# Kernel optimization log

Measured on AMD Instinct MI355X. Metric: run time of the kernel, lower is better.

## Reference

```python
import jax, jax.numpy as jnp
import numpy as np

N = 20000      # nodes
E = 160000     # edges (before self loops)
F = 256        # num_features
HID = 64       # hidden_channels
H = 4          # num_heads
HC = HID // H  # head channels = 16
C = 10         # num_classes
K = 3          # hops
ALPHA = 0.1
CST = 1e-5


def setup_inputs() -> dict:
    key = jax.random.key(0)
    ks = jax.random.split(key, 12)
    node_feat = jax.random.normal(ks[0], (N, F), dtype=jnp.float32)
    edge_index = jax.random.randint(ks[1], (2, E), 0, N, dtype=jnp.int32)

    def lin(k, fan_in, fan_out):
        b = 1.0 / np.sqrt(fan_in)
        kw, kb = jax.random.split(k)
        W = jax.random.uniform(kw, (fan_in, fan_out), jnp.float32, -b, b)
        bias = jax.random.uniform(kb, (fan_out,), jnp.float32, -b, b)
        return W, bias

    W_in, b_in = lin(ks[2], F, HID)
    Wq, bq = lin(ks[3], HID, H * HC)
    Wk, bk = lin(ks[4], HID, H * HC)
    Wv, bv = lin(ks[5], HID, H * C)
    W_out, b_out = lin(ks[6], H * C, C)

    # hopwise: alpha*(1-alpha)^k, last entry (1-alpha)^K
    hw = ALPHA * (1 - ALPHA) ** np.arange(K + 1, dtype=np.float32)
    hw[-1] = (1 - ALPHA) ** K
    hopwise = jnp.asarray(hw, dtype=jnp.float32)
    # temp: uniform one-head vector normalized by L1, tiled per head
    bound = np.sqrt(3.0 / (K + 1))
    onehead = jax.random.uniform(ks[7], (K + 1,), jnp.float32, -bound, bound)
    onehead = onehead / jnp.sum(jnp.abs(onehead))
    temp = jnp.tile(onehead[None, :], (H, 1))  # [H, K+1]

    return dict(node_feat=node_feat, edge_index=edge_index, W_in=W_in, b_in=b_in,
                Wq=Wq, bq=bq, Wk=Wk, bk=bk, Wv=Wv, bv=bv,
                W_out=W_out, b_out=b_out, hopwise=hopwise, temp=temp)


def reference(node_feat, edge_index, W_in, b_in, Wq, bq, Wk, bk, Wv, bv,
              W_out, b_out, hopwise, temp):
    # add self loops
    loops = jnp.arange(N, dtype=edge_index.dtype)
    ei = jnp.concatenate([edge_index, jnp.stack([loops, loops])], axis=1)
    row, col = ei[0], ei[1]
    # symmetric-normalized laplacian weights
    deg = jnp.zeros((N,), node_feat.dtype).at[col].add(1.0)
    dis = jnp.where(deg > 0, 1.0 / jnp.sqrt(jnp.maximum(deg, 1.0)), 0.0)
    norm = dis[row] * dis[col]  # [E+N]

    x = jax.nn.relu(node_feat @ W_in + b_in)                      # [N, HID]
    Q = (1.0 + jax.nn.elu(x @ Wq + bq)).reshape(N, H, HC)
    Kt = (1.0 + jax.nn.elu(x @ Wk + bk)).reshape(N, H, HC)
    V = (x @ Wv + bv).reshape(N, H, C)

    M = jnp.einsum('nhi,nhj->nhij', Kt, V)                        # [N, H, HC, C]
    hidden = V * hopwise[0]
    # NOTE: faithful to torch: softmax over dim=-2 of temp [H, K+1] == head axis
    layerwise = jax.nn.softmax(temp, axis=0)                      # [H, K+1]

    for hop in range(K):
        M = jax.ops.segment_sum(norm[:, None, None, None] * M[row], col, num_segments=N)
        Kt = jax.ops.segment_sum(norm[:, None, None] * Kt[row], col, num_segments=N)
        Hh = jnp.einsum('nhi,nhij->nhj', Q, M)                    # [N, H, C]
        Cd = jnp.einsum('nhi,nhi->nh', Q, Kt)[..., None] + CST    # [N, H, 1]
        gamma = hopwise[hop + 1] * layerwise[:, hop + 1][:, None]  # [H, 1]
        hidden = hidden + gamma * (Hh / Cd)

    out = hidden.reshape(N, H * C) @ W_out + b_out                # [N, C]
    return out
```

## Files before the change

### kernel.cpp

```cpp
#include <hip/hip_runtime.h>
#include <stdint.h>

#define kN   20000
#define kE   160000
#define kET  (kN + kE)
#define kF   256
#define kHID 64
#define kH   4
#define kHC  16
#define kC   10
#define kK   3
#define kCST 1e-5f
#define kBN  32
#define kNB  ((kN + 255) / 256)

__device__ __forceinline__ uint16_t f2bf(float x) {
    uint32_t u = __float_as_uint(x);
    u += 0x7fffu + ((u >> 16) & 1u);
    return (uint16_t)(u >> 16);
}
__device__ __forceinline__ float lo16(uint32_t p) { return __uint_as_float(p << 16); }
__device__ __forceinline__ float hi16(uint32_t p) { return __uint_as_float(p & 0xffff0000u); }
__device__ __forceinline__ uint32_t pack2(float a, float b) {
    return ((uint32_t)f2bf(b) << 16) | (uint32_t)f2bf(a);
}

__global__ void deg_kernel(const int* __restrict__ ei, int* __restrict__ deg) {
    int e = blockIdx.x * blockDim.x + threadIdx.x;
    if (e >= kET) return;
    int c = (e < kE) ? ei[kE + e] : (e - kE);
    atomicAdd(&deg[c], 1);
}

__global__ __launch_bounds__(256) void degsum_kernel(const int* __restrict__ deg,
                                                     int* __restrict__ partial) {
    __shared__ int sw[4];
    int t = threadIdx.x;
    int idx = blockIdx.x * 256 + t;
    int v = (idx < kN) ? deg[idx] : 0;
#pragma unroll
    for (int off = 32; off >= 1; off >>= 1) v += __shfl_xor(v, off, 64);
    if ((t & 63) == 0) sw[t >> 6] = v;
    __syncthreads();
    if (t == 0) partial[blockIdx.x] = sw[0] + sw[1] + sw[2] + sw[3];
}

__global__ __launch_bounds__(128) void midscan_kernel(
    const int* __restrict__ partial, int* __restrict__ offsets,
    const float* __restrict__ hopwise, const float* __restrict__ temp,
    float* __restrict__ gammas) {
    __shared__ int ws0;
    int t = threadIdx.x;
    int v = (t < kNB) ? partial[t] : 0;
    int incl = v;
#pragma unroll
    for (int off = 1; off < 64; off <<= 1) {
        int u = __shfl_up(incl, off, 64);
        if ((t & 63) >= off) incl += u;
    }
    if (t == 63) ws0 = incl;
    __syncthreads();
    int add = (t >= 64) ? ws0 : 0;
    if (t < kNB) offsets[t] = add + incl - v;
    if (t == 0) {
        for (int k = 1; k <= kK; ++k) {
            float mx = -1e30f;
            for (int h = 0; h < kH; ++h) mx = fmaxf(mx, temp[h * (kK + 1) + k]);
            float ex[kH]; float sum = 0.f;
            for (int h = 0; h < kH; ++h) { ex[h] = __expf(temp[h * (kK + 1) + k] - mx); sum += ex[h]; }
            for (int h = 0; h < kH; ++h) gammas[(k - 1) * kH + h] = hopwise[k] * ex[h] / sum;
        }
    }
}

__global__ __launch_bounds__(256) void ptrw_kernel(const int* __restrict__ deg,
                                                   const int* __restrict__ offsets,
                                                   int* __restrict__ ptr) {
    __shared__ int sw[4];
    int t = threadIdx.x;
    int idx = blockIdx.x * 256 + t;
    int v = (idx < kN) ? deg[idx] : 0;
    int incl = v;
#pragma unroll
    for (int off = 1; off < 64; off <<= 1) {
        int u = __shfl_up(incl, off, 64);
        if ((t & 63) >= off) incl += u;
    }
    int wid = t >> 6;
    if ((t & 63) == 63) sw[wid] = incl;
    __syncthreads();
    int wadd = 0;
    for (int j = 0; j < 4; ++j) wadd += (j < wid) ? sw[j] : 0;
    int excl = offsets[blockIdx.x] + wadd + incl - v;
    if (idx < kN) ptr[idx] = excl;
    if (idx == kN - 1) ptr[kN] = excl + v;
}

__global__ void scatter_kernel(const int* __restrict__ ei, const int* __restrict__ deg,
                               const int* __restrict__ ptr, int* __restrict__ cursor,
                               int* __restrict__ src, float* __restrict__ wgt) {
    int e = blockIdx.x * blockDim.x + threadIdx.x;
    if (e >= kET) return;
    int r, c;
    if (e < kE) { r = ei[e]; c = ei[kE + e]; } else { r = c = e - kE; }
    float wv = rsqrtf((float)deg[r]) * rsqrtf((float)deg[c]);
    int pos = ptr[c] + atomicAdd(&cursor[c], 1);
    src[pos] = r;
    wgt[pos] = wv;
}

__global__ __launch_bounds__(256) void proj_kernel(
    const float* __restrict__ feat, const float* __restrict__ W_in, const float* __restrict__ b_in,
    const float* __restrict__ Wq, const float* __restrict__ bq,
    const float* __restrict__ Wk, const float* __restrict__ bk,
    const float* __restrict__ Wv, const float* __restrict__ bv,
    const float* __restrict__ hopwise,
    float* __restrict__ Qg, float* __restrict__ Ktg, float* __restrict__ hidden,
    float* __restrict__ Vg) {
    __shared__ float sF[kBN * 68];
    __shared__ float sW[64 * 68];
    __shared__ float sX[kBN * 68];

    int t = threadIdx.x;
    int tx = t & 15, ty = t >> 4;
    int n0 = blockIdx.x * kBN;
    int r0 = ty * 2, r1 = ty * 2 + 1;

    float acc[2][4];
#pragma unroll
    for (int i = 0; i < 2; ++i)
#pragma unroll
        for (int j = 0; j < 4; ++j) acc[i][j] = 0.f;

    for (int ks = 0; ks < 4; ++ks) {
        int k0 = ks * 64;
#pragma unroll
        for (int i = 0; i < 2; ++i) {
            int slot = t + 256 * i;
            int row = slot >> 4, cg = slot & 15;
            *(float4*)&sF[row * 68 + cg * 4] =
                *(const float4*)&feat[(size_t)(n0 + row) * kF + k0 + cg * 4];
        }
#pragma unroll
        for (int i = 0; i < 4; ++i) {
            int slot = t + 256 * i;
            int row = slot >> 4, cg = slot & 15;
            *(float4*)&sW[row * 68 + cg * 4] =
                *(const float4*)&W_in[(size_t)(k0 + row) * kHID + cg * 4];
        }
        __syncthreads();
#pragma unroll 8
        for (int kk = 0; kk < 64; ++kk) {
            float4 b = *(float4*)&sW[kk * 68 + tx * 4];
            float a0 = sF[r0 * 68 + kk], a1 = sF[r1 * 68 + kk];
            acc[0][0] += a0 * b.x; acc[0][1] += a0 * b.y;
            acc[0][2] += a0 * b.z; acc[0][3] += a0 * b.w;
            acc[1][0] += a1 * b.x; acc[1][1] += a1 * b.y;
            acc[1][2] += a1 * b.z; acc[1][3] += a1 * b.w;
        }
        __syncthreads();
    }
    {
        float bb[4];
#pragma unroll
        for (int j = 0; j < 4; ++j) bb[j] = b_in[tx * 4 + j];
#pragma unroll
        for (int i = 0; i < 2; ++i) {
            float4 xr;
            xr.x = fmaxf(acc[i][0] + bb[0], 0.f);
            xr.y = fmaxf(acc[i][1] + bb[1], 0.f);
            xr.z = fmaxf(acc[i][2] + bb[2], 0.f);
            xr.w = fmaxf(acc[i][3] + bb[3], 0.f);
            *(float4*)&sX[(r0 + i) * 68 + tx * 4] = xr;
        }
    }
#pragma unroll
    for (int i = 0; i < 4; ++i) {
        int slot = t + 256 * i;
        int row = slot >> 4, cg = slot & 15;
        *(float4*)&sW[row * 68 + cg * 4] = *(const float4*)&Wq[(size_t)row * kHID + cg * 4];
    }
    __syncthreads();

    float qa[2][4];
#pragma unroll
    for (int i = 0; i < 2; ++i)
#pragma unroll
        for (int j = 0; j < 4; ++j) qa[i][j] = 0.f;
#pragma unroll 8
    for (int kk = 0; kk < 64; ++kk) {
        float4 b = *(float4*)&sW[kk * 68 + tx * 4];
        float a0 = sX[r0 * 68 + kk], a1 = sX[r1 * 68 + kk];
        qa[0][0] += a0 * b.x; qa[0][1] += a0 * b.y;
        qa[0][2] += a0 * b.z; qa[0][3] += a0 * b.w;
        qa[1][0] += a1 * b.x; qa[1][1] += a1 * b.y;
        qa[1][2] += a1 * b.z; qa[1][3] += a1 * b.w;
    }
    {
        float bqv[4];
#pragma unroll
        for (int j = 0; j < 4; ++j) bqv[j] = bq[tx * 4 + j];
#pragma unroll
        for (int i = 0; i < 2; ++i) {
            float4 qv;
            float q0 = qa[i][0] + bqv[0], q1 = qa[i][1] + bqv[1];
            float q2 = qa[i][2] + bqv[2], q3 = qa[i][3] + bqv[3];
            qv.x = (q0 > 0.f) ? 1.f + q0 : __expf(q0);
            qv.y = (q1 > 0.f) ? 1.f + q1 : __expf(q1);
            qv.z = (q2 > 0.f) ? 1.f + q2 : __expf(q2);
            qv.w = (q3 > 0.f) ? 1.f + q3 : __expf(q3);
            *(float4*)&Qg[(size_t)(n0 + r0 + i) * kHID + tx * 4] = qv;
        }
    }
    __syncthreads();
#pragma unroll
    for (int i = 0; i < 4; ++i) {
        int slot = t + 256 * i;
        int row = slot >> 4, cg = slot & 15;
        *(float4*)&sW[row * 68 + cg * 4] = *(const float4*)&Wk[(size_t)row * kHID + cg * 4];
    }
    __syncthreads();

    float ka[2][4];
#pragma unroll
    for (int i = 0; i < 2; ++i)
#pragma unroll
        for (int j = 0; j < 4; ++j) ka[i][j] = 0.f;
#pragma unroll 8
    for (int kk = 0; kk < 64; ++kk) {
        float4 b = *(float4*)&sW[kk * 68 + tx * 4];
        float a0 = sX[r0 * 68 + kk], a1 = sX[r1 * 68 + kk];
        ka[0][0] += a0 * b.x; ka[0][1] += a0 * b.y;
        ka[0][2] += a0 * b.z; ka[0][3] += a0 * b.w;
        ka[1][0] += a1 * b.x; ka[1][1] += a1 * b.y;
        ka[1][2] += a1 * b.z; ka[1][3] += a1 * b.w;
    }
    {
        float bkv[4];
#pragma unroll
        for (int j = 0; j < 4; ++j) bkv[j] = bk[tx * 4 + j];
#pragma unroll
        for (int i = 0; i < 2; ++i) {
            float4 kv;
            float k0v = ka[i][0] + bkv[0], k1v = ka[i][1] + bkv[1];
            float k2v = ka[i][2] + bkv[2], k3v = ka[i][3] + bkv[3];
            kv.x = (k0v > 0.f) ? 1.f + k0v : __expf(k0v);
            kv.y = (k1v > 0.f) ? 1.f + k1v : __expf(k1v);
            kv.z = (k2v > 0.f) ? 1.f + k2v : __expf(k2v);
            kv.w = (k3v > 0.f) ? 1.f + k3v : __expf(k3v);
            *(float4*)&Ktg[(size_t)(n0 + r0 + i) * kHID + tx * 4] = kv;
        }
    }
    __syncthreads();
#pragma unroll
    for (int i = 0; i < 3; ++i) {
        int slot = t + 256 * i;
        if (slot < 640) {
            int row = slot / 10, cg = slot % 10;
            *(float4*)&sW[row * 44 + cg * 4] = *(const float4*)&Wv[(size_t)row * 40 + cg * 4];
        }
    }
    __syncthreads();

    if (t < 160) {
        int txv = t % 10, tyv = t / 10;
        int vr0 = tyv * 2;
        float va[2][4];
#pragma unroll
        for (int i = 0; i < 2; ++i)
#pragma unroll
            for (int j = 0; j < 4; ++j) va[i][j] = 0.f;
#pragma unroll 8
        for (int kk = 0; kk < 64; ++kk) {
            float4 b = *(float4*)&sW[kk * 44 + txv * 4];
            float a0 = sX[vr0 * 68 + kk], a1 = sX[(vr0 + 1) * 68 + kk];
            va[0][0] += a0 * b.x; va[0][1] += a0 * b.y;
            va[0][2] += a0 * b.z; va[0][3] += a0 * b.w;
            va[1][0] += a1 * b.x; va[1][1] += a1 * b.y;
            va[1][2] += a1 * b.z; va[1][3] += a1 * b.w;
        }
        float bvv[4];
#pragma unroll
        for (int j = 0; j < 4; ++j) bvv[j] = bv[txv * 4 + j];
        float hw0 = hopwise[0];
#pragma unroll
        for (int i = 0; i < 2; ++i) {
            int row = vr0 + i;
            float4 vr;
            vr.x = va[i][0] + bvv[0]; vr.y = va[i][1] + bvv[1];
            vr.z = va[i][2] + bvv[2]; vr.w = va[i][3] + bvv[3];
            *(float4*)&Vg[(size_t)(n0 + row) * 40 + txv * 4] = vr;
            float4 hr;
            hr.x = vr.x * hw0; hr.y = vr.y * hw0; hr.z = vr.z * hw0; hr.w = vr.w * hw0;
            *(float4*)&hidden[(size_t)(n0 + row) * 40 + txv * 4] = hr;
        }
    }
}

__global__ __launch_bounds__(256) void hop0_kernel(
    const int* __restrict__ ptr, const int* __restrict__ src, const float* __restrict__ wgt,
    const float* __restrict__ Ktin, const float* __restrict__ Vin,
    const float* __restrict__ Q,
    uint16_t* __restrict__ Mout, float* __restrict__ Ktout,
    float* __restrict__ hidden, const float* __restrict__ gammas) {
    __shared__ float Ml[4][640];
    __shared__ float Ktl[4][64];
    __shared__ float Ql[4][64];
    int w = threadIdx.x >> 6;
    int l = threadIdx.x & 63;
    int n = blockIdx.x * 4 + w;
    int beg = ptr[n], end = ptr[n + 1];

    Ql[w][l] = Q[(size_t)n * 64 + l];

    int base_v = 10 * (l >> 4);
    int vidx = (l < 40) ? l : l - 40;

    float m[10];
#pragma unroll
    for (int i = 0; i < 10; ++i) m[i] = 0.f;
    float kacc = 0.f;

    auto edge = [&](float kl, float vv, float wv) {
        float kw = wv * kl;
        kacc += wv * kl;
#pragma unroll
        for (int c = 0; c < 10; ++c) {
            float vc = __shfl(vv, base_v + c, 64);
            m[c] += kw * vc;
        }
    };

    int e = beg;
    for (; e + 4 <= end; e += 4) {
        int s0 = src[e], s1 = src[e + 1], s2 = src[e + 2], s3 = src[e + 3];
        float w0 = wgt[e], w1 = wgt[e + 1], w2 = wgt[e + 2], w3 = wgt[e + 3];
        float ka = Ktin[(size_t)s0 * 64 + l], va = Vin[(size_t)s0 * 40 + vidx];
        float kb = Ktin[(size_t)s1 * 64 + l], vb = Vin[(size_t)s1 * 40 + vidx];
        float kc = Ktin[(size_t)s2 * 64 + l], vc = Vin[(size_t)s2 * 40 + vidx];
        float kd = Ktin[(size_t)s3 * 64 + l], vd = Vin[(size_t)s3 * 40 + vidx];
        edge(ka, va, w0); edge(kb, vb, w1); edge(kc, vc, w2); edge(kd, vd, w3);
    }
    for (; e < end; ++e) {
        int s0 = src[e];
        edge(Ktin[(size_t)s0 * 64 + l], Vin[(size_t)s0 * 40 + vidx], wgt[e]);
    }

    {
        uint32_t* orow = (uint32_t*)Mout + (size_t)n * 320 + 5 * l;
        orow[0] = pack2(m[0], m[1]);
        orow[1] = pack2(m[2], m[3]);
        orow[2] = pack2(m[4], m[5]);
        orow[3] = pack2(m[6], m[7]);
        orow[4] = pack2(m[8], m[9]);
        Ktout[(size_t)n * 64 + l] = kacc;
    }
#pragma unroll
    for (int c = 0; c < 10; c += 2)
        *(float2*)&Ml[w][10 * l + c] = make_float2(m[c], m[c + 1]);
    Ktl[w][l] = kacc;
    __syncthreads();

    int tt = threadIdx.x;
    if (tt < 160) {
        int ww = tt / 40, o = tt % 40;
        int h = o / 10, j = o % 10;
        const float* q  = &Ql[ww][h * 16];
        const float* kk = &Ktl[ww][h * 16];
        const float* mm = &Ml[ww][h * 160 + j];
        float cd = kCST, hh = 0.f;
#pragma unroll
        for (int i = 0; i < 16; ++i) { cd += q[i] * kk[i]; hh += q[i] * mm[i * 10]; }
        int nn = blockIdx.x * 4 + ww;
        hidden[(size_t)nn * 40 + o] += gammas[h] * hh / cd;
    }
}

template<bool LAST>
__global__ __launch_bounds__(256) void hop2_kernel(
    const int* __restrict__ ptr, const int* __restrict__ src, const float* __restrict__ wgt,
    const uint16_t* __restrict__ Min, uint16_t* __restrict__ Mout,
    const float* __restrict__ Ktin, float* __restrict__ Ktout,
    const float* __restrict__ Q, float* __restrict__ hidden,
    const float* __restrict__ gammas,
    const float* __restrict__ W_out, const float* __restrict__ b_out,
    float* __restrict__ out) {
    __shared__ float Ml[4][640];
    __shared__ float Ktl[4][64];
    __shared__ float Ql[4][64];
    __shared__ float Hl[4][40];
    int w = threadIdx.x >> 6;
    int l = threadIdx.x & 63;
    int n = blockIdx.x * 4 + w;
    int beg = ptr[n], end = ptr[n + 1];
    const uint32_t* Mw = (const uint32_t*)Min;

    Ql[w][l] = Q[(size_t)n * 64 + l];

    float m0=0,m1=0,m2=0,m3=0,m4=0,m5=0,m6=0,m7=0,m8=0,m9=0;
    float kacc = 0.f;
    int e = beg;
    for (; e + 4 <= end; e += 4) {
        int s0 = src[e], s1 = src[e + 1], s2 = src[e + 2], s3 = src[e + 3];
        float w0 = wgt[e], w1 = wgt[e + 1], w2 = wgt[e + 2], w3 = wgt[e + 3];
        const uint32_t* p0 = Mw + (size_t)s0 * 320 + l;
        const uint32_t* p1 = Mw + (size_t)s1 * 320 + l;
        const uint32_t* p2 = Mw + (size_t)s2 * 320 + l;
        const uint32_t* p3 = Mw + (size_t)s3 * 320 + l;
        uint32_t a0 = p0[0], a1 = p0[64], a2 = p0[128], a3 = p0[192], a4 = p0[256];
        uint32_t b0 = p1[0], b1 = p1[64], b2 = p1[128], b3 = p1[192], b4 = p1[256];
        uint32_t c0 = p2[0], c1 = p2[64], c2 = p2[128], c3 = p2[192], c4 = p2[256];
        uint32_t d0 = p3[0], d1 = p3[64], d2 = p3[128], d3 = p3[192], d4 = p3[256];
        float ka = Ktin[(size_t)s0 * 64 + l], kb = Ktin[(size_t)s1 * 64 + l];
        float kc = Ktin[(size_t)s2 * 64 + l], kd = Ktin[(size_t)s3 * 64 + l];
        m0 += w0 * lo16(a0); m1 += w0 * hi16(a0);
        m2 += w0 * lo16(a1); m3 += w0 * hi16(a1);
        m4 += w0 * lo16(a2); m5 += w0 * hi16(a2);
        m6 += w0 * lo16(a3); m7 += w0 * hi16(a3);
        m8 += w0 * lo16(a4); m9 += w0 * hi16(a4);
        m0 += w1 * lo16(b0); m1 += w1 * hi16(b0);
        m2 += w1 * lo16(b1); m3 += w1 * hi16(b1);
        m4 += w1 * lo16(b2); m5 += w1 * hi16(b2);
        m6 += w1 * lo16(b3); m7 += w1 * hi16(b3);
        m8 += w1 * lo16(b4); m9 += w1 * hi16(b4);
        m0 += w2 * lo16(c0); m1 += w2 * hi16(c0);
        m2 += w2 * lo16(c1); m3 += w2 * hi16(c1);
        m4 += w2 * lo16(c2); m5 += w2 * hi16(c2);
        m6 += w2 * lo16(c3); m7 += w2 * hi16(c3);
        m8 += w2 * lo16(c4); m9 += w2 * hi16(c4);
        m0 += w3 * lo16(d0); m1 += w3 * hi16(d0);
        m2 += w3 * lo16(d1); m3 += w3 * hi16(d1);
        m4 += w3 * lo16(d2); m5 += w3 * hi16(d2);
        m6 += w3 * lo16(d3); m7 += w3 * hi16(d3);
        m8 += w3 * lo16(d4); m9 += w3 * hi16(d4);
        kacc += w0 * ka + w1 * kb + w2 * kc + w3 * kd;
    }
    for (; e + 2 <= end; e += 2) {
        int s0 = src[e], s1 = src[e + 1];
        float w0 = wgt[e], w1 = wgt[e + 1];
        const uint32_t* p0 = Mw + (size_t)s0 * 320 + l;
        const uint32_t* p1 = Mw + (size_t)s1 * 320 + l;
        uint32_t a0 = p0[0], a1 = p0[64], a2 = p0[128], a3 = p0[192], a4 = p0[256];
        uint32_t b0 = p1[0], b1 = p1[64], b2 = p1[128], b3 = p1[192], b4 = p1[256];
        float ka = Ktin[(size_t)s0 * 64 + l], kb = Ktin[(size_t)s1 * 64 + l];
        m0 += w0 * lo16(a0); m1 += w0 * hi16(a0);
        m2 += w0 * lo16(a1); m3 += w0 * hi16(a1);
        m4 += w0 * lo16(a2); m5 += w0 * hi16(a2);
        m6 += w0 * lo16(a3); m7 += w0 * hi16(a3);
        m8 += w0 * lo16(a4); m9 += w0 * hi16(a4);
        m0 += w1 * lo16(b0); m1 += w1 * hi16(b0);
        m2 += w1 * lo16(b1); m3 += w1 * hi16(b1);
        m4 += w1 * lo16(b2); m5 += w1 * hi16(b2);
        m6 += w1 * lo16(b3); m7 += w1 * hi16(b3);
        m8 += w1 * lo16(b4); m9 += w1 * hi16(b4);
        kacc += w0 * ka + w1 * kb;
    }
    if (e < end) {
        int s0 = src[e];
        float w0 = wgt[e];
        const uint32_t* p0 = Mw + (size_t)s0 * 320 + l;
        uint32_t a0 = p0[0], a1 = p0[64], a2 = p0[128], a3 = p0[192], a4 = p0[256];
        float ka = Ktin[(size_t)s0 * 64 + l];
        m0 += w0 * lo16(a0); m1 += w0 * hi16(a0);
        m2 += w0 * lo16(a1); m3 += w0 * hi16(a1);
        m4 += w0 * lo16(a2); m5 += w0 * hi16(a2);
        m6 += w0 * lo16(a3); m7 += w0 * hi16(a3);
        m8 += w0 * lo16(a4); m9 += w0 * hi16(a4);
        kacc += w0 * ka;
    }

    *(float2*)&Ml[w][2 * l]         = make_float2(m0, m1);
    *(float2*)&Ml[w][2 * (l + 64)]  = make_float2(m2, m3);
    *(float2*)&Ml[w][2 * (l + 128)] = make_float2(m4, m5);
    *(float2*)&Ml[w][2 * (l + 192)] = make_float2(m6, m7);
    *(float2*)&Ml[w][2 * (l + 256)] = make_float2(m8, m9);
    Ktl[w][l] = kacc;
    if constexpr (!LAST) {
        uint32_t* orow = (uint32_t*)Mout + (size_t)n * 320 + l;
        orow[0]   = pack2(m0, m1);
        orow[64]  = pack2(m2, m3);
        orow[128] = pack2(m4, m5);
        orow[192] = pack2(m6, m7);
        orow[256] = pack2(m8, m9);
        Ktout[(size_t)n * 64 + l] = kacc;
    }
    __syncthreads();

    int tt = threadIdx.x;
    if (tt < 160) {
        int ww = tt / 40, o = tt % 40;
        int h = o / 10, j = o % 10;
        const float* q  = &Ql[ww][h * 16];
        const float* kk = &Ktl[ww][h * 16];
        const float* mm = &Ml[ww][h * 160 + j];
        float cd = kCST, hh = 0.f;
#pragma unroll
        for (int i = 0; i < 16; ++i) { cd += q[i] * kk[i]; hh += q[i] * mm[i * 10]; }
        int nn = blockIdx.x * 4 + ww;
        float val = hidden[(size_t)nn * 40 + o] + gammas[h] * hh / cd;
        if constexpr (!LAST) hidden[(size_t)nn * 40 + o] = val;
        else Hl[ww][o] = val;
    }
    if constexpr (LAST) {
        __syncthreads();
        if (tt < 40) {
            int ww = tt / 10, c = tt % 10;
            float acc = b_out[c];
#pragma unroll
            for (int i = 0; i < 40; ++i) acc += Hl[ww][i] * W_out[i * 10 + c];
            out[(size_t)(blockIdx.x * 4 + ww) * 10 + c] = acc;
        }
    }
}

extern "C" void kernel_launch(void* const* d_in, const int* in_sizes, int n_in,
                              void* d_out, int out_size, void* d_ws, size_t ws_size,
                              hipStream_t stream) {
    const float* feat   = (const float*)d_in[0];
    const int*   ei     = (const int*)d_in[1];
    const float* W_in   = (const float*)d_in[2];
    const float* b_in   = (const float*)d_in[3];
    const float* Wq     = (const float*)d_in[4];
    const float* bq     = (const float*)d_in[5];
    const float* Wk     = (const float*)d_in[6];
    const float* bk     = (const float*)d_in[7];
    const float* Wv     = (const float*)d_in[8];
    const float* bv     = (const float*)d_in[9];
    const float* W_out  = (const float*)d_in[10];
    const float* b_out  = (const float*)d_in[11];
    const float* hopwise= (const float*)d_in[12];
    const float* temp   = (const float*)d_in[13];
    float* out = (float*)d_out;

    char* ws = (char*)d_ws;
    size_t off = 0;
    auto alloc = [&](size_t bytes) -> void* {
        void* p = ws + off;
        off += (bytes + 255) & ~(size_t)255;
        return p;
    };
    int*      deg    = (int*)alloc((size_t)kN * 4);
    int*      cursor = (int*)alloc((size_t)kN * 4);
    int*      ptr    = (int*)alloc((size_t)(kN + 1) * 4);
    int*      partial= (int*)alloc((size_t)kNB * 4);
    int*      offs   = (int*)alloc((size_t)kNB * 4);
    int*      csrc   = (int*)alloc((size_t)kET * 4);
    float*    cwgt   = (float*)alloc((size_t)kET * 4);
    float*    Q      = (float*)alloc((size_t)kN * kHID * 4);
    float*    Kt0    = (float*)alloc((size_t)kN * kHID * 4);
    float*    Kt1    = (float*)alloc((size_t)kN * kHID * 4);
    float*    Vg     = (float*)alloc((size_t)kN * kH * kC * 4);
    float*    hidden = (float*)alloc((size_t)kN * kH * kC * 4);
    float*    gammas = (float*)alloc(64);
    uint16_t* M1     = (uint16_t*)alloc((size_t)kN * 640 * 2);
    uint16_t* M2     = (uint16_t*)alloc((size_t)kN * 640 * 2);
    (void)ws_size; (void)in_sizes; (void)n_in; (void)out_size;

    size_t deg_span = (size_t)((char*)cursor - (char*)deg) + (size_t)kN * 4;
    hipMemsetAsync(deg, 0, deg_span, stream);

    deg_kernel<<<(kET + 255) / 256, 256, 0, stream>>>(ei, deg);
    degsum_kernel<<<kNB, 256, 0, stream>>>(deg, partial);
    midscan_kernel<<<1, 128, 0, stream>>>(partial, offs, hopwise, temp, gammas);
    ptrw_kernel<<<kNB, 256, 0, stream>>>(deg, offs, ptr);
    scatter_kernel<<<(kET + 255) / 256, 256, 0, stream>>>(ei, deg, ptr, cursor, csrc, cwgt);
    proj_kernel<<<kN / kBN, 256, 0, stream>>>(feat, W_in, b_in, Wq, bq, Wk, bk, Wv, bv,
                                              hopwise, Q, Kt0, hidden, Vg);
    hop0_kernel<<<kN / 4, 256, 0, stream>>>(ptr, csrc, cwgt, Kt0, Vg, Q, M1, Kt1, hidden,
                                            gammas + 0);
    hop2_kernel<false><<<kN / 4, 256, 0, stream>>>(ptr, csrc, cwgt, M1, M2, Kt1, Kt0, Q, hidden,
                                                   gammas + 4, W_out, b_out, out);
    hop2_kernel<true><<<kN / 4, 256, 0, stream>>>(ptr, csrc, cwgt, M2, M1, Kt0, Kt1, Q, hidden,
                                                  gammas + 8, W_out, b_out, out);
}
```

Measured before the change: 176.7 us.

## Split hop M/Kt state into eight interleaved slices with per-slice gather kernels

```diff
diff --git a/kernel.cpp b/kernel.cpp
--- a/kernel.cpp
+++ b/kernel.cpp
@@ -13,6 +13,7 @@
 #define kCST 1e-5f
 #define kBN  32
 #define kNB  ((kN + 255) / 256)
+#define kMS  ((size_t)kN * 48)
 
 __device__ __forceinline__ uint16_t f2bf(float x) {
     uint32_t u = __float_as_uint(x);
@@ -301,7 +302,7 @@
     const int* __restrict__ ptr, const int* __restrict__ src, const float* __restrict__ wgt,
     const float* __restrict__ Ktin, const float* __restrict__ Vin,
     const float* __restrict__ Q,
-    uint16_t* __restrict__ Mout, float* __restrict__ Ktout,
+    uint32_t* __restrict__ Mout,
     float* __restrict__ hidden, const float* __restrict__ gammas) {
     __shared__ float Ml[4][640];
     __shared__ float Ktl[4][64];
@@ -347,13 +348,15 @@
     }
 
     {
-        uint32_t* orow = (uint32_t*)Mout + (size_t)n * 320 + 5 * l;
+        int p = l >> 3, r = l & 7;
+        uint32_t* row = Mout + (size_t)p * kMS + (size_t)n * 48;
+        uint32_t* orow = row + r * 5;
         orow[0] = pack2(m[0], m[1]);
         orow[1] = pack2(m[2], m[3]);
         orow[2] = pack2(m[4], m[5]);
         orow[3] = pack2(m[6], m[7]);
         orow[4] = pack2(m[8], m[9]);
-        Ktout[(size_t)n * 64 + l] = kacc;
+        row[40 + r] = __float_as_uint(kacc);
     }
 #pragma unroll
     for (int c = 0; c < 10; c += 2)
@@ -377,138 +380,121 @@
 }
 
 template<bool LAST>
-__global__ __launch_bounds__(256) void hop2_kernel(
+__global__ __launch_bounds__(256) void shop_kernel(
     const int* __restrict__ ptr, const int* __restrict__ src, const float* __restrict__ wgt,
-    const uint16_t* __restrict__ Min, uint16_t* __restrict__ Mout,
-    const float* __restrict__ Ktin, float* __restrict__ Ktout,
-    const float* __restrict__ Q, float* __restrict__ hidden,
-    const float* __restrict__ gammas,
+    const uint32_t* __restrict__ Msrc, uint32_t* __restrict__ Mdst,
+    const float* __restrict__ Q,
+    float* __restrict__ HhBuf, float* __restrict__ CdBuf) {
+    __shared__ float Qs[4][8];
+    __shared__ float st[4][88];
+    int t = threadIdx.x;
+    int w = t >> 6, l = t & 63;
+    int b = blockIdx.x;
+    int p = b & 7, g = b >> 3;
+    int n = g * 4 + w;
+    int eo = l >> 3, r = l & 7;
+    int beg = ptr[n], end = ptr[n + 1];
+    const uint32_t* Mp = Msrc + (size_t)p * kMS;
+
+    int h = p >> 1, ib = (p & 1) << 3;
+    if (l < 8) Qs[w][l] = Q[(size_t)n * 64 + h * 16 + ib + l];
+
+    float ml[5], mh[5];
+#pragma unroll
+    for (int k = 0; k < 5; ++k) { ml[k] = 0.f; mh[k] = 0.f; }
+    float kt = 0.f;
+
+    for (int e = beg; e < end; e += 8) {
+        int ee = e + eo;
+        if (ee < end) {
+            int su = __builtin_nontemporal_load(&src[ee]);
+            float wv = __builtin_nontemporal_load(&wgt[ee]);
+            const uint32_t* row = Mp + (size_t)su * 48 + r;
+            uint32_t a0 = row[0], a1 = row[8], a2 = row[16], a3 = row[24], a4 = row[32];
+            uint32_t kv = row[40];
+            ml[0] += wv * lo16(a0); mh[0] += wv * hi16(a0);
+            ml[1] += wv * lo16(a1); mh[1] += wv * hi16(a1);
+            ml[2] += wv * lo16(a2); mh[2] += wv * hi16(a2);
+            ml[3] += wv * lo16(a3); mh[3] += wv * hi16(a3);
+            ml[4] += wv * lo16(a4); mh[4] += wv * hi16(a4);
+            kt += wv * __uint_as_float(kv);
+        }
+    }
+#pragma unroll
+    for (int msk = 8; msk <= 32; msk <<= 1) {
+#pragma unroll
+        for (int k = 0; k < 5; ++k) {
+            ml[k] += __shfl_xor(ml[k], msk, 64);
+            mh[k] += __shfl_xor(mh[k], msk, 64);
+        }
+        kt += __shfl_xor(kt, msk, 64);
+    }
+
+    if constexpr (!LAST) {
+        if (l < 40) {
+            float lo = (eo == 0) ? ml[0] : (eo == 1) ? ml[1] : (eo == 2) ? ml[2]
+                     : (eo == 3) ? ml[3] : ml[4];
+            float hi = (eo == 0) ? mh[0] : (eo == 1) ? mh[1] : (eo == 2) ? mh[2]
+                     : (eo == 3) ? mh[3] : mh[4];
+            __builtin_nontemporal_store(pack2(lo, hi),
+                &Mdst[(size_t)p * kMS + (size_t)n * 48 + l]);
+        } else if (l < 48) {
+            __builtin_nontemporal_store(__float_as_uint(kt),
+                &Mdst[(size_t)p * kMS + (size_t)n * 48 + l]);
+        }
+    }
+    if (l < 8) {
+#pragma unroll
+        for (int k = 0; k < 5; ++k) {
+            st[w][2 * (r + 8 * k)]     = ml[k];
+            st[w][2 * (r + 8 * k) + 1] = mh[k];
+        }
+        st[w][80 + r] = kt;
+    }
+    if (l < 10) {
+        float hh = 0.f;
+#pragma unroll
+        for (int i = 0; i < 8; ++i) hh += Qs[w][i] * st[w][i * 10 + l];
+        __builtin_nontemporal_store(hh, &HhBuf[((size_t)n * 8 + p) * 10 + l]);
+    } else if (l == 10) {
+        float cd = 0.f;
+#pragma unroll
+        for (int i = 0; i < 8; ++i) cd += Qs[w][i] * st[w][80 + i];
+        __builtin_nontemporal_store(cd, &CdBuf[(size_t)n * 8 + p]);
+    }
+}
+
+template<bool LAST>
+__global__ __launch_bounds__(256) void epi_kernel(
+    const float* __restrict__ HhBuf, const float* __restrict__ CdBuf,
+    const float* __restrict__ gam, float* __restrict__ hidden,
     const float* __restrict__ W_out, const float* __restrict__ b_out,
     float* __restrict__ out) {
-    __shared__ float Ml[4][640];
-    __shared__ float Ktl[4][64];
-    __shared__ float Ql[4][64];
-    __shared__ float Hl[4][40];
-    int w = threadIdx.x >> 6;
-    int l = threadIdx.x & 63;
-    int n = blockIdx.x * 4 + w;
-    int beg = ptr[n], end = ptr[n + 1];
-    const uint32_t* Mw = (const uint32_t*)Min;
-
-    Ql[w][l] = Q[(size_t)n * 64 + l];
-
-    float m0=0,m1=0,m2=0,m3=0,m4=0,m5=0,m6=0,m7=0,m8=0,m9=0;
-    float kacc = 0.f;
-    int e = beg;
-    for (; e + 4 <= end; e += 4) {
-        int s0 = src[e], s1 = src[e + 1], s2 = src[e + 2], s3 = src[e + 3];
-        float w0 = wgt[e], w1 = wgt[e + 1], w2 = wgt[e + 2], w3 = wgt[e + 3];
-        const uint32_t* p0 = Mw + (size_t)s0 * 320 + l;
-        const uint32_t* p1 = Mw + (size_t)s1 * 320 + l;
-        const uint32_t* p2 = Mw + (size_t)s2 * 320 + l;
-        const uint32_t* p3 = Mw + (size_t)s3 * 320 + l;
-        uint32_t a0 = p0[0], a1 = p0[64], a2 = p0[128], a3 = p0[192], a4 = p0[256];
-        uint32_t b0 = p1[0], b1 = p1[64], b2 = p1[128], b3 = p1[192], b4 = p1[256];
-        uint32_t c0 = p2[0], c1 = p2[64], c2 = p2[128], c3 = p2[192], c4 = p2[256];
-        uint32_t d0 = p3[0], d1 = p3[64], d2 = p3[128], d3 = p3[192], d4 = p3[256];
-        float ka = Ktin[(size_t)s0 * 64 + l], kb = Ktin[(size_t)s1 * 64 + l];
-        float kc = Ktin[(size_t)s2 * 64 + l], kd = Ktin[(size_t)s3 * 64 + l];
-        m0 += w0 * lo16(a0); m1 += w0 * hi16(a0);
-        m2 += w0 * lo16(a1); m3 += w0 * hi16(a1);
-        m4 += w0 * lo16(a2); m5 += w0 * hi16(a2);
-        m6 += w0 * lo16(a3); m7 += w0 * hi16(a3);
-        m8 += w0 * lo16(a4); m9 += w0 * hi16(a4);
-        m0 += w1 * lo16(b0); m1 += w1 * hi16(b0);
-        m2 += w1 * lo16(b1); m3 += w1 * hi16(b1);
-        m4 += w1 * lo16(b2); m5 += w1 * hi16(b2);
-        m6 += w1 * lo16(b3); m7 += w1 * hi16(b3);
-        m8 += w1 * lo16(b4); m9 += w1 * hi16(b4);
-        m0 += w2 * lo16(c0); m1 += w2 * hi16(c0);
-        m2 += w2 * lo16(c1); m3 += w2 * hi16(c1);
-        m4 += w2 * lo16(c2); m5 += w2 * hi16(c2);
-        m6 += w2 * lo16(c3); m7 += w2 * hi16(c3);
-        m8 += w2 * lo16(c4); m9 += w2 * hi16(c4);
-        m0 += w3 * lo16(d0); m1 += w3 * hi16(d0);
-        m2 += w3 * lo16(d1); m3 += w3 * hi16(d1);
-        m4 += w3 * lo16(d2); m5 += w3 * hi16(d2);
-        m6 += w3 * lo16(d3); m7 += w3 * hi16(d3);
-        m8 += w3 * lo16(d4); m9 += w3 * hi16(d4);
-        kacc += w0 * ka + w1 * kb + w2 * kc + w3 * kd;
-    }
-    for (; e + 2 <= end; e += 2) {
-        int s0 = src[e], s1 = src[e + 1];
-        float w0 = wgt[e], w1 = wgt[e + 1];
-        const uint32_t* p0 = Mw + (size_t)s0 * 320 + l;
-        const uint32_t* p1 = Mw + (size_t)s1 * 320 + l;
-        uint32_t a0 = p0[0], a1 = p0[64], a2 = p0[128], a3 = p0[192], a4 = p0[256];
-        uint32_t b0 = p1[0], b1 = p1[64], b2 = p1[128], b3 = p1[192], b4 = p1[256];
-        float ka = Ktin[(size_t)s0 * 64 + l], kb = Ktin[(size_t)s1 * 64 + l];
-        m0 += w0 * lo16(a0); m1 += w0 * hi16(a0);
-        m2 += w0 * lo16(a1); m3 += w0 * hi16(a1);
-        m4 += w0 * lo16(a2); m5 += w0 * hi16(a2);
-        m6 += w0 * lo16(a3); m7 += w0 * hi16(a3);
-        m8 += w0 * lo16(a4); m9 += w0 * hi16(a4);
-        m0 += w1 * lo16(b0); m1 += w1 * hi16(b0);
-        m2 += w1 * lo16(b1); m3 += w1 * hi16(b1);
-        m4 += w1 * lo16(b2); m5 += w1 * hi16(b2);
-        m6 += w1 * lo16(b3); m7 += w1 * hi16(b3);
-        m8 += w1 * lo16(b4); m9 += w1 * hi16(b4);
-        kacc += w0 * ka + w1 * kb;
-    }
-    if (e < end) {
-        int s0 = src[e];
-        float w0 = wgt[e];
-        const uint32_t* p0 = Mw + (size_t)s0 * 320 + l;
-        uint32_t a0 = p0[0], a1 = p0[64], a2 = p0[128], a3 = p0[192], a4 = p0[256];
-        float ka = Ktin[(size_t)s0 * 64 + l];
-        m0 += w0 * lo16(a0); m1 += w0 * hi16(a0);
-        m2 += w0 * lo16(a1); m3 += w0 * hi16(a1);
-        m4 += w0 * lo16(a2); m5 += w0 * hi16(a2);
-        m6 += w0 * lo16(a3); m7 += w0 * hi16(a3);
-        m8 += w0 * lo16(a4); m9 += w0 * hi16(a4);
-        kacc += w0 * ka;
-    }
-
-    *(float2*)&Ml[w][2 * l]         = make_float2(m0, m1);
-    *(float2*)&Ml[w][2 * (l + 64)]  = make_float2(m2, m3);
-    *(float2*)&Ml[w][2 * (l + 128)] = make_float2(m4, m5);
-    *(float2*)&Ml[w][2 * (l + 192)] = make_float2(m6, m7);
-    *(float2*)&Ml[w][2 * (l + 256)] = make_float2(m8, m9);
-    Ktl[w][l] = kacc;
-    if constexpr (!LAST) {
-        uint32_t* orow = (uint32_t*)Mout + (size_t)n * 320 + l;
-        orow[0]   = pack2(m0, m1);
-        orow[64]  = pack2(m2, m3);
-        orow[128] = pack2(m4, m5);
-        orow[192] = pack2(m6, m7);
-        orow[256] = pack2(m8, m9);
-        Ktout[(size_t)n * 64 + l] = kacc;
-    }
-    __syncthreads();
-
-    int tt = threadIdx.x;
-    if (tt < 160) {
-        int ww = tt / 40, o = tt % 40;
-        int h = o / 10, j = o % 10;
-        const float* q  = &Ql[ww][h * 16];
-        const float* kk = &Ktl[ww][h * 16];
-        const float* mm = &Ml[ww][h * 160 + j];
-        float cd = kCST, hh = 0.f;
-#pragma unroll
-        for (int i = 0; i < 16; ++i) { cd += q[i] * kk[i]; hh += q[i] * mm[i * 10]; }
-        int nn = blockIdx.x * 4 + ww;
-        float val = hidden[(size_t)nn * 40 + o] + gammas[h] * hh / cd;
-        if constexpr (!LAST) hidden[(size_t)nn * 40 + o] = val;
-        else Hl[ww][o] = val;
+    __shared__ float Hl[6][40];
+    int t = threadIdx.x;
+    int node = blockIdx.x * 6 + t / 40;
+    int o = t % 40;
+    bool act = (t < 240) && (node < kN);
+    if (act) {
+        int h = o / 10, j = o - h * 10;
+        float hh = HhBuf[(size_t)node * 80 + (2 * h) * 10 + j]
+                 + HhBuf[(size_t)node * 80 + (2 * h + 1) * 10 + j];
+        float cd = CdBuf[(size_t)node * 8 + 2 * h] + CdBuf[(size_t)node * 8 + 2 * h + 1] + kCST;
+        float val = hidden[(size_t)node * 40 + o] + gam[h] * hh / cd;
+        if constexpr (!LAST) hidden[(size_t)node * 40 + o] = val;
+        else Hl[t / 40][o] = val;
     }
     if constexpr (LAST) {
         __syncthreads();
-        if (tt < 40) {
-            int ww = tt / 10, c = tt % 10;
-            float acc = b_out[c];
-#pragma unroll
-            for (int i = 0; i < 40; ++i) acc += Hl[ww][i] * W_out[i * 10 + c];
-            out[(size_t)(blockIdx.x * 4 + ww) * 10 + c] = acc;
+        if (t < 60) {
+            int s = t / 10, c = t - s * 10;
+            int nn = blockIdx.x * 6 + s;
+            if (nn < kN) {
+                float acc = b_out[c];
+#pragma unroll
+                for (int i = 0; i < 40; ++i) acc += Hl[s][i] * W_out[i * 10 + c];
+                out[(size_t)nn * 10 + c] = acc;
+            }
         }
     }
 }
@@ -548,12 +534,13 @@
     float*    cwgt   = (float*)alloc((size_t)kET * 4);
     float*    Q      = (float*)alloc((size_t)kN * kHID * 4);
     float*    Kt0    = (float*)alloc((size_t)kN * kHID * 4);
-    float*    Kt1    = (float*)alloc((size_t)kN * kHID * 4);
     float*    Vg     = (float*)alloc((size_t)kN * kH * kC * 4);
     float*    hidden = (float*)alloc((size_t)kN * kH * kC * 4);
     float*    gammas = (float*)alloc(64);
-    uint16_t* M1     = (uint16_t*)alloc((size_t)kN * 640 * 2);
-    uint16_t* M2     = (uint16_t*)alloc((size_t)kN * 640 * 2);
+    float*    HhBuf  = (float*)alloc((size_t)kN * 80 * 4);
+    float*    CdBuf  = (float*)alloc((size_t)kN * 8 * 4);
+    uint32_t* Ms1    = (uint32_t*)alloc((size_t)8 * kMS * 4);
+    uint32_t* Ms2    = (uint32_t*)alloc((size_t)8 * kMS * 4);
     (void)ws_size; (void)in_sizes; (void)n_in; (void)out_size;
 
     size_t deg_span = (size_t)((char*)cursor - (char*)deg) + (size_t)kN * 4;
@@ -566,10 +553,12 @@
     scatter_kernel<<<(kET + 255) / 256, 256, 0, stream>>>(ei, deg, ptr, cursor, csrc, cwgt);
     proj_kernel<<<kN / kBN, 256, 0, stream>>>(feat, W_in, b_in, Wq, bq, Wk, bk, Wv, bv,
                                               hopwise, Q, Kt0, hidden, Vg);
-    hop0_kernel<<<kN / 4, 256, 0, stream>>>(ptr, csrc, cwgt, Kt0, Vg, Q, M1, Kt1, hidden,
+    hop0_kernel<<<kN / 4, 256, 0, stream>>>(ptr, csrc, cwgt, Kt0, Vg, Q, Ms1, hidden,
                                             gammas + 0);
-    hop2_kernel<false><<<kN / 4, 256, 0, stream>>>(ptr, csrc, cwgt, M1, M2, Kt1, Kt0, Q, hidden,
-                                                   gammas + 4, W_out, b_out, out);
-    hop2_kernel<true><<<kN / 4, 256, 0, stream>>>(ptr, csrc, cwgt, M2, M1, Kt0, Kt1, Q, hidden,
-                                                  gammas + 8, W_out, b_out, out);
-}
+    const int SG = (kN / 4) * 8;
+    const int EG = (kN + 5) / 6;
+    shop_kernel<false><<<SG, 256, 0, stream>>>(ptr, csrc, cwgt, Ms1, Ms2, Q, HhBuf, CdBuf);
+    epi_kernel<false><<<EG, 256, 0, stream>>>(HhBuf, CdBuf, gammas + 4, hidden, W_out, b_out, out);
+    shop_kernel<true><<<SG, 256, 0, stream>>>(ptr, csrc, cwgt, Ms2, Ms1, Q, HhBuf, CdBuf);
+    epi_kernel<true><<<EG, 256, 0, stream>>>(HhBuf, CdBuf, gammas + 8, hidden, W_out, b_out, out);
+}
```

After: 288.3 us. 1.63x slower.
